# Optimization experiments

Measured on AMD Instinct MI355X. Metric: run time of the kernel, lower is better.

The kernel has to match this reference:

```python
import jax, jax.numpy as jnp
import numpy as np
from jax import lax

HEADS = 8
DIM_HEAD = 64
INNER = HEADS * DIM_HEAD  # 512
DIM = 256
TOP_K = 512  # top_k=-1 -> Lk // heads = 4096 // 8
LN_EPS = 1e-5


def chan_ln(x, g, b):
    # LayerNorm over channel dim (axis=1) of [b,c,D,H,W]
    mu = jnp.mean(x, axis=1, keepdims=True)
    var = jnp.mean((x - mu) ** 2, axis=1, keepdims=True)
    xn = (x - mu) * lax.rsqrt(var + LN_EPS)
    return xn * g[None, :, None, None, None] + b[None, :, None, None, None]


def l1_cdist(K, Q):
    # K: [B,N,D], Q: [B,M,D] -> [B,N,M]; scan over feature dim to avoid a [B,N,M,D] intermediate
    Kt = jnp.moveaxis(K, -1, 0)  # [D,B,N]
    Qt = jnp.moveaxis(Q, -1, 0)  # [D,B,M]
    acc0 = jnp.zeros((K.shape[0], K.shape[1], Q.shape[1]), K.dtype)
    def step(acc, kq):
        kd, qd = kq
        return acc + jnp.abs(kd[:, :, None] - qd[:, None, :]), None
    acc, _ = lax.scan(step, acc0, (Kt, Qt))
    return acc


def l2norm_ax(t, axis):
    n = jnp.sqrt(jnp.sum(t * t, axis=axis, keepdims=True))
    return t / jnp.maximum(n, 1e-12)


def setup_inputs() -> dict:
    key = jax.random.key(0)
    ks = jax.random.split(key, 12)
    b, Dq, Hq, Wq = 2, 16, 32, 32
    Dc, Hc, Wc = 16, 16, 16
    Lk = Dc * Hc * Wc  # 4096
    return {
        "query_source": jax.random.normal(ks[0], (b, DIM, Dq, Hq, Wq), jnp.float32),
        "context": jax.random.normal(ks[1], (b, DIM, Dc, Hc, Wc), jnp.float32),
        "rand_idx": jax.random.randint(ks[2], (b * HEADS, TOP_K), 0, 4096),
        "g_ctx": jnp.ones((DIM,), jnp.float32),
        "b_ctx": jnp.zeros((DIM,), jnp.float32),
        "g_qs": jnp.ones((DIM,), jnp.float32),
        "b_qs": jnp.zeros((DIM,), jnp.float32),
        "w_kv": jax.random.normal(ks[3], (2 * INNER, DIM), jnp.float32) * 0.02,
        "w_q": jax.random.normal(ks[4], (INNER, DIM), jnp.float32) * 0.02,
        "w_out": jax.random.normal(ks[5], (DIM, INNER), jnp.float32) * 0.02,
        "g_out": jnp.ones((DIM,), jnp.float32),
        "b_out": jnp.zeros((DIM,), jnp.float32),
        "gamma": jnp.full((1,), 0.5, jnp.float32),
    }


def reference(query_source, context, rand_idx, g_ctx, b_ctx, g_qs, b_qs,
              w_kv, w_q, w_out, g_out, b_out, gamma):
    b, c, Dq, Hq, Wq = query_source.shape
    Lq = Dq * Hq * Wq
    Lk = context.shape[2] * context.shape[3] * context.shape[4]

    ctx = chan_ln(context, g_ctx, b_ctx)
    qsn = chan_ln(query_source, g_qs, b_qs)

    # 1x1x1 convs == channel matmuls
    kv = jnp.einsum('oc,bcdhw->bodhw', w_kv, ctx)
    k, v = jnp.split(kv, 2, axis=1)
    q = jnp.einsum('oc,bcdhw->bodhw', w_q, qsn)

    def fold(t):  # [b, inner, ...] -> [b, heads, dim_head, L]
        return t.reshape(t.shape[0], HEADS, DIM_HEAD, -1)
    q, k, v = fold(q), fold(k), fold(v)
    # l2norm over dim_head channels (torch dim=1 after (b h) fold)
    q = l2norm_ax(q, 2)
    k = l2norm_ax(k, 2)
    # -> [b, heads, L, dim_head]
    q = jnp.swapaxes(q, 2, 3)
    k = jnp.swapaxes(k, 2, 3)
    v = jnp.swapaxes(v, 2, 3)

    BH = b * HEADS
    qf = q.reshape(BH, Lq, DIM_HEAD)
    kf = k.reshape(BH, Lk, DIM_HEAD)
    vf = v.reshape(BH, Lk, DIM_HEAD)

    # random-query-anchored token pruning
    Q_small = jnp.take_along_axis(qf, rand_idx[:, :, None], axis=1)  # [BH, TOP_K, dh]
    dist = l1_cdist(kf, Q_small)                                     # [BH, Lk, TOP_K]
    min_d = jnp.min(dist, axis=2)                                    # [BH, Lk]
    _, idx = lax.top_k(-min_d, TOP_K)                                # smallest distances
    ks_sel = jnp.take_along_axis(kf, idx[:, :, None], axis=1)        # [BH, TOP_K, dh]
    vs_sel = jnp.take_along_axis(vf, idx[:, :, None], axis=1)

    ks4 = ks_sel.reshape(b, HEADS, TOP_K, DIM_HEAD)
    vs4 = vs_sel.reshape(b, HEADS, TOP_K, DIM_HEAD)

    # SDPA with scale=1.0, no dropout (eval)
    scores = jnp.einsum('bhqd,bhkd->bhqk', q, ks4)
    attn = jax.nn.softmax(scores, axis=-1)
    out = jnp.einsum('bhqk,bhkd->bhqd', attn, vs4)  # [b,H,Lq,dh]

    out = out.reshape(b, HEADS, Dq, Hq, Wq, DIM_HEAD)
    out = jnp.transpose(out, (0, 1, 5, 2, 3, 4)).reshape(b, INNER, Dq, Hq, Wq)
    out = jnp.einsum('oc,bcdhw->bodhw', w_out, out)
    out = chan_ln(out, g_out, b_out)
    return gamma[0] * out + query_source
```

## Files before the change

### kernel.cpp

```cpp
#include <hip/hip_runtime.h>
#include <hip/hip_bf16.h>
#include <math.h>

#define DIMC  256
#define HEADS 8
#define DH    64
#define INNER 512
#define TOPK  512
#define LQ    16384
#define LKE   4096
#define NB    2
#define NBH   16

typedef __attribute__((ext_vector_type(8))) short bf16x8;
typedef __attribute__((ext_vector_type(4))) float f32x4;
typedef __attribute__((ext_vector_type(16))) unsigned u32x16;

__device__ __forceinline__ unsigned short f2bf(float f) {
    unsigned u = __float_as_uint(f);
    u += 0x7FFFu + ((u >> 16) & 1u);
    return (unsigned short)(u >> 16);
}
__device__ __forceinline__ float bf2f(unsigned short b) {
    return __uint_as_float(((unsigned)b) << 16);
}
__device__ __forceinline__ f32x4 mfma16(bf16x8 a, bf16x8 b, f32x4 c) {
    return __builtin_amdgcn_mfma_f32_16x16x32_bf16(a, b, c, 0, 0, 0);
}
__device__ __forceinline__ unsigned f2q16(float v) {
    return (unsigned)((int)rintf(v * 32000.0f) + 32768) & 0xFFFFu;
}

__global__ void stats_kernel(const float* __restrict__ x, float* __restrict__ mu,
                             float* __restrict__ rs, int L, int total) {
    int idx = blockIdx.x * 256 + threadIdx.x;
    if (idx >= total) return;
    int b = idx / L, l = idx - b * L;
    const float* p = x + (size_t)b * DIMC * L + l;
    float s = 0.f, sq = 0.f;
    for (int c = 0; c < DIMC; c++) {
        float v = p[(size_t)c * L];
        s += v; sq += v * v;
    }
    float m = s * (1.0f / DIMC);
    float var = fmaxf(sq * (1.0f / DIMC) - m * m, 0.f);
    mu[idx] = m;
    rs[idx] = rsqrtf(var + 1e-5f);
}

template<bool WRITELO>
__global__ __launch_bounds__(256) void ln_transpose_kernel(
    const float* __restrict__ x, const float* __restrict__ mu, const float* __restrict__ rs,
    const float* __restrict__ g, const float* __restrict__ beta, int L,
    unsigned short* __restrict__ xhi, unsigned short* __restrict__ xlo) {
    int lt = blockIdx.x, ct = blockIdx.y, b = blockIdx.z;
    int l0 = lt * 64, c0 = ct * 64;
    int t = threadIdx.x;
    __shared__ float T[64][65];
#pragma unroll
    for (int r = 0; r < 16; r++) {
        int f = r * 256 + t;
        int l = f & 63, c = f >> 6;
        int loc = b * L + l0 + l;
        float v = x[((size_t)b * DIMC + c0 + c) * L + l0 + l];
        T[c][l] = (v - mu[loc]) * rs[loc] * g[c0 + c] + beta[c0 + c];
    }
    __syncthreads();
#pragma unroll
    for (int r = 0; r < 16; r++) {
        int f = r * 256 + t;
        int c = f & 63, l = f >> 6;
        float v = T[c][l];
        unsigned short hi = f2bf(v);
        size_t di = ((size_t)b * L + l0 + l) * DIMC + c0 + c;
        xhi[di] = hi;
        if (WRITELO) xlo[di] = f2bf(v - bf2f(hi));
    }
}

template<int MODE>
__global__ __launch_bounds__(256) void gemm_mfma_kernel(
    const float* __restrict__ wmat,
    const unsigned short* __restrict__ xhi, const unsigned short* __restrict__ xlo,
    void* __restrict__ dst0, void* __restrict__ dst1, void* __restrict__ dst2) {
    constexpr int K = (MODE == 2) ? 512 : 256;
    constexpr int N = (MODE == 0) ? LKE : LQ;
    constexpr bool MAYSPLIT = (MODE == 0);
    int n0 = blockIdx.x * 128;
    int by = blockIdx.y;
    int bb = blockIdx.z;
    int t = threadIdx.x, w = t >> 6, lane = t & 63;
    int wm = w >> 1, wn = w & 1;
    int lanelo = lane & 15, lanehi = lane >> 4;

    __shared__ __align__(16) char Wh[16384];
    __shared__ __align__(16) char Xh[16384];
    __shared__ __align__(16) char Wl[MAYSPLIT ? 16384 : 16];
    __shared__ __align__(16) char Xl[MAYSPLIT ? 16384 : 16];

    bool split = MAYSPLIT && (by < 4);

    const float* wsrc = wmat + (size_t)by * 128 * K;
    const unsigned short* xsh = xhi + ((size_t)bb * N + n0) * K;
    const unsigned short* xsl = xlo + ((size_t)bb * N + n0) * K;

    f32x4 acc[4][4];
#pragma unroll
    for (int mi = 0; mi < 4; mi++)
#pragma unroll
        for (int ni = 0; ni < 4; ni++) acc[mi][ni] = (f32x4){0.f, 0.f, 0.f, 0.f};

    for (int k0 = 0; k0 < K; k0 += 64) {
        if (k0) __syncthreads();
#pragma unroll
        for (int gg = 0; gg < 4; gg++) {
            int e = gg * 2048 + t * 8;
            int row = e >> 6, kc = e & 63;
            const float* wp = wsrc + (size_t)row * K + k0 + kc;
            bf16x8 hi, lo;
#pragma unroll
            for (int i = 0; i < 8; i++) {
                float v = wp[i];
                unsigned short h = f2bf(v);
                hi[i] = (short)h;
                if (MAYSPLIT) lo[i] = (short)f2bf(v - bf2f(h));
            }
            int off = (row * 128 + kc * 2) ^ ((row & 7) << 4);
            *(bf16x8*)(Wh + off) = hi;
            *(bf16x8*)(Xh + off) = *(const bf16x8*)(xsh + (size_t)row * K + k0 + kc);
            if (split) {
                *(bf16x8*)(Wl + off) = lo;
                *(bf16x8*)(Xl + off) = *(const bf16x8*)(xsl + (size_t)row * K + k0 + kc);
            }
        }
        __syncthreads();
#pragma unroll
        for (int kk = 0; kk < 2; kk++) {
            bf16x8 ah[4], bh_[4];
#pragma unroll
            for (int mi = 0; mi < 4; mi++) {
                int row = wm * 64 + mi * 16 + lanelo;
                int off = (row * 128 + kk * 64 + lanehi * 16) ^ ((row & 7) << 4);
                ah[mi] = *(const bf16x8*)(Wh + off);
            }
#pragma unroll
            for (int ni = 0; ni < 4; ni++) {
                int row = wn * 64 + ni * 16 + lanelo;
                int off = (row * 128 + kk * 64 + lanehi * 16) ^ ((row & 7) << 4);
                bh_[ni] = *(const bf16x8*)(Xh + off);
            }
#pragma unroll
            for (int mi = 0; mi < 4; mi++)
#pragma unroll
                for (int ni = 0; ni < 4; ni++)
                    acc[mi][ni] = mfma16(ah[mi], bh_[ni], acc[mi][ni]);
            if (split) {
                bf16x8 al[4], bl_[4];
#pragma unroll
                for (int mi = 0; mi < 4; mi++) {
                    int row = wm * 64 + mi * 16 + lanelo;
                    int off = (row * 128 + kk * 64 + lanehi * 16) ^ ((row & 7) << 4);
                    al[mi] = *(const bf16x8*)(Wl + off);
                }
#pragma unroll
                for (int ni = 0; ni < 4; ni++) {
                    int row = wn * 64 + ni * 16 + lanelo;
                    int off = (row * 128 + kk * 64 + lanehi * 16) ^ ((row & 7) << 4);
                    bl_[ni] = *(const bf16x8*)(Xl + off);
                }
#pragma unroll
                for (int mi = 0; mi < 4; mi++)
#pragma unroll
                    for (int ni = 0; ni < 4; ni++) {
                        acc[mi][ni] = mfma16(ah[mi], bl_[ni], acc[mi][ni]);
                        acc[mi][ni] = mfma16(al[mi], bh_[ni], acc[mi][ni]);
                    }
            }
        }
    }

    bool donorm = (MODE == 1) || (MODE == 0 && by < 4);
    float inv[4];
    if (donorm) {
#pragma unroll
        for (int ni = 0; ni < 4; ni++) {
            float s = 0.f;
#pragma unroll
            for (int mi = 0; mi < 4; mi++)
#pragma unroll
                for (int rg = 0; rg < 4; rg++) s += acc[mi][ni][rg] * acc[mi][ni][rg];
            s += __shfl_xor(s, 16);
            s += __shfl_xor(s, 32);
            inv[ni] = 1.0f / fmaxf(sqrtf(s), 1e-12f);
        }
    }
#pragma unroll
    for (int mi = 0; mi < 4; mi++) {
        int rowg = by * 128 + wm * 64 + mi * 16 + lanehi * 4;
#pragma unroll
        for (int ni = 0; ni < 4; ni++) {
            int l = n0 + wn * 64 + ni * 16 + lanelo;
            if (MODE == 0) {
                bool isk = rowg < 512;
                float sc = isk ? inv[ni] : 1.0f;
                int h = (rowg >> 6) & 7, d0 = rowg & 63;
                float4 v = make_float4(acc[mi][ni][0] * sc, acc[mi][ni][1] * sc,
                                       acc[mi][ni][2] * sc, acc[mi][ni][3] * sc);
                float* dp = isk ? (float*)dst0 : (float*)dst1;
                size_t base = ((size_t)(bb * HEADS + h) * LKE + l) * 64 + d0;
                *(float4*)&dp[base] = v;
                if (isk) {
                    uint2 pk;
                    pk.x = f2q16(v.x) | (f2q16(v.y) << 16);
                    pk.y = f2q16(v.z) | (f2q16(v.w) << 16);
                    *(uint2*)&((unsigned*)dst2)[(((size_t)(bb * HEADS + h) * LKE + l) * 64 + d0) / 2] = pk;
                }
            } else if (MODE == 1) {
                int h = rowg >> 6, d0 = rowg & 63;
                ushort4 u;
                u.x = f2bf(acc[mi][ni][0] * inv[ni]);
                u.y = f2bf(acc[mi][ni][1] * inv[ni]);
                u.z = f2bf(acc[mi][ni][2] * inv[ni]);
                u.w = f2bf(acc[mi][ni][3] * inv[ni]);
                unsigned short* qp = (unsigned short*)dst0;
                *(ushort4*)&qp[((size_t)(bb * HEADS + h) * LQ + l) * 64 + d0] = u;
            } else {
                float4 v = make_float4(acc[mi][ni][0], acc[mi][ni][1],
                                       acc[mi][ni][2], acc[mi][ni][3]);
                float* pp = (float*)dst0;
                *(float4*)&pp[((size_t)bb * LQ + l) * 256 + rowg] = v;
            }
        }
    }
}

__global__ __launch_bounds__(256) void qsample_kernel(
    const float* __restrict__ x, const float* __restrict__ mu, const float* __restrict__ rs,
    const float* __restrict__ g, const float* __restrict__ beta,
    const float* __restrict__ w, const int* __restrict__ ridx,
    unsigned* __restrict__ Qint) {
    int lt = blockIdx.x, bh = blockIdx.y;
    int b = bh >> 3, h = bh & 7;
    int t = threadIdx.x, tx = t & 15, ty = t >> 4;
    __shared__ float Ws[64][33];
    __shared__ float Xs[32][65];
    __shared__ float Cs[64][65];
    __shared__ float nf[64];
    __shared__ int lidx[64];
    if (t < 64) lidx[t] = ridx[bh * TOPK + lt * 64 + t];
    __syncthreads();
    float acc[4][4];
#pragma unroll
    for (int a = 0; a < 4; a++)
#pragma unroll
        for (int c2 = 0; c2 < 4; c2++) acc[a][c2] = 0.f;
    for (int kc = 0; kc < DIMC; kc += 32) {
#pragma unroll
        for (int r = 0; r < 8; r++) {
            int f = r * 256 + t;
            int oi = f >> 5, kj = f & 31;
            Ws[oi][kj] = w[(size_t)(h * 64 + oi) * DIMC + kc + kj];
        }
#pragma unroll
        for (int r = 0; r < 8; r++) {
            int f = r * 256 + t;
            int kj = f >> 6, lj = f & 63;
            int l = lidx[lj];
            int loc = b * LQ + l;
            float v = x[(size_t)b * DIMC * LQ + (size_t)(kc + kj) * LQ + l];
            Xs[kj][lj] = (v - mu[loc]) * rs[loc] * g[kc + kj] + beta[kc + kj];
        }
        __syncthreads();
#pragma unroll
        for (int kj = 0; kj < 32; kj++) {
            float wr[4], xr[4];
#pragma unroll
            for (int a = 0; a < 4; a++) wr[a] = Ws[ty * 4 + a][kj];
#pragma unroll
            for (int c2 = 0; c2 < 4; c2++) xr[c2] = Xs[kj][tx * 4 + c2];
#pragma unroll
            for (int a = 0; a < 4; a++)
#pragma unroll
                for (int c2 = 0; c2 < 4; c2++) acc[a][c2] += wr[a] * xr[c2];
        }
        __syncthreads();
    }
#pragma unroll
    for (int a = 0; a < 4; a++)
#pragma unroll
        for (int c2 = 0; c2 < 4; c2++) Cs[ty * 4 + a][tx * 4 + c2] = acc[a][c2];
    __syncthreads();
    if (t < 64) {
        float sq = 0.f;
        for (int o = 0; o < 64; o++) { float v = Cs[o][t]; sq += v * v; }
        nf[t] = 1.0f / fmaxf(sqrtf(sq), 1e-12f);
    }
    __syncthreads();
#pragma unroll
    for (int r = 0; r < 8; r++) {
        int f = r * 256 + t;
        int dp = f & 31, lj = f >> 5;
        float v0 = Cs[dp * 2][lj] * nf[lj];
        float v1 = Cs[dp * 2 + 1][lj] * nf[lj];
        Qint[((size_t)bh * TOPK + (size_t)lt * 64 + lj) * 32 + dp] =
            f2q16(v0) | (f2q16(v1) << 16);
    }
}

__global__ __launch_bounds__(256) __attribute__((amdgpu_waves_per_eu(4, 4)))
void cdist_sad_kernel(
    const unsigned* __restrict__ kint,
    const unsigned* __restrict__ Qint,
    unsigned* __restrict__ min_d4) {
    int bh = blockIdx.y;
    int key = blockIdx.x * 256 + threadIdx.x;
    int qz = blockIdx.z;
    const unsigned* kp = kint + ((size_t)bh * LKE + key) * 32;
    unsigned k[32];
#pragma unroll
    for (int d8 = 0; d8 < 8; d8++) {
        uint4 v = *(const uint4*)(kp + d8 * 4);
        k[d8 * 4 + 0] = v.x; k[d8 * 4 + 1] = v.y;
        k[d8 * 4 + 2] = v.z; k[d8 * 4 + 3] = v.w;
    }
#pragma unroll
    for (int d = 0; d < 32; d++) asm volatile("" : "+v"(k[d]));

    unsigned long long qaddr = (unsigned long long)(const void*)
        (Qint + ((size_t)bh * TOPK + (size_t)qz * (TOPK / 4)) * 32);
    u32x16 qa0, qa1, qb0, qb1;
    asm volatile(
        "s_load_dwordx16 %0, %2, 0x00\n\t"
        "s_load_dwordx16 %1, %2, 0x40"
        : "=s"(qa0), "=s"(qa1) : "s"(qaddr));
    unsigned best = 0xFFFFFFFFu;

#define S1(ACC, KK, QQ) asm("v_sad_u16 %0, %1, %2, %0" : "+v"(ACC) : "v"(KK), "s"(QQ));
#define S16(QV, KB) \
    S1(a0, k[KB + 0], QV[0])  S1(a1, k[KB + 1], QV[1]) \
    S1(a2, k[KB + 2], QV[2])  S1(a3, k[KB + 3], QV[3]) \
    S1(a0, k[KB + 4], QV[4])  S1(a1, k[KB + 5], QV[5]) \
    S1(a2, k[KB + 6], QV[6])  S1(a3, k[KB + 7], QV[7]) \
    S1(a0, k[KB + 8], QV[8])  S1(a1, k[KB + 9], QV[9]) \
    S1(a2, k[KB + 10], QV[10]) S1(a3, k[KB + 11], QV[11]) \
    S1(a0, k[KB + 12], QV[12]) S1(a1, k[KB + 13], QV[13]) \
    S1(a2, k[KB + 14], QV[14]) S1(a3, k[KB + 15], QV[15])

    for (int qi = 0; qi < TOPK / 4; qi += 2) {
        asm volatile(
            "s_load_dwordx16 %0, %2, 0x80\n\t"
            "s_load_dwordx16 %1, %2, 0xc0"
            : "=s"(qb0), "=s"(qb1) : "s"(qaddr));
        asm volatile("s_waitcnt lgkmcnt(2)" : "+s"(qa0), "+s"(qa1));
        {
            unsigned a0 = 0, a1 = 0, a2 = 0, a3 = 0;
            S16(qa0, 0) S16(qa1, 16)
            best = min(best, (a0 + a1) + (a2 + a3));
        }
        qaddr += 256;
        asm volatile(
            "s_load_dwordx16 %0, %2, 0x00\n\t"
            "s_load_dwordx16 %1, %2, 0x40"
            : "=s"(qa0), "=s"(qa1) : "s"(qaddr));
        asm volatile("s_waitcnt lgkmcnt(2)" : "+s"(qb0), "+s"(qb1));
        {
            unsigned a0 = 0, a1 = 0, a2 = 0, a3 = 0;
            S16(qb0, 0) S16(qb1, 16)
            best = min(best, (a0 + a1) + (a2 + a3));
        }
    }
#undef S16
#undef S1
    min_d4[((size_t)qz * NBH + bh) * LKE + key] = best;
}

__global__ void select_topk_kernel(const unsigned* __restrict__ min_d4, int* __restrict__ isel) {
    int bh = blockIdx.x;
    int t = threadIdx.x;
    __shared__ unsigned su[LKE];
    __shared__ int hist[256];
    __shared__ int sb[2];
    for (int i = t; i < LKE; i += 256) {
        unsigned a = min(min_d4[(size_t)bh * LKE + i],
                         min_d4[(size_t)(NBH + bh) * LKE + i]);
        unsigned b = min(min_d4[(size_t)(2 * NBH + bh) * LKE + i],
                         min_d4[(size_t)(3 * NBH + bh) * LKE + i]);
        su[i] = min(a, b);
    }
    unsigned prefix = 0, mask = 0;
    int need = TOPK;
    for (int shift = 24; shift >= 0; shift -= 8) {
        hist[t] = 0;
        __syncthreads();
        for (int i = t; i < LKE; i += 256) {
            unsigned u = su[i];
            if ((u & mask) == prefix) atomicAdd(&hist[(u >> shift) & 255], 1);
        }
        __syncthreads();
        if (t == 0) {
            int c = 0, bsel = 0;
            for (; bsel < 255; bsel++) {
                if (c + hist[bsel] >= need) break;
                c += hist[bsel];
            }
            sb[0] = bsel; sb[1] = need - c;
        }
        __syncthreads();
        prefix |= ((unsigned)sb[0]) << shift;
        mask |= (255u << shift);
        need = sb[1];
        __syncthreads();
    }
    if (t < 64) {
        int pos = 0, eqseen = 0;
        unsigned long long lanem1 = (t == 0) ? 0ull : ((1ull << t) - 1ull);
        for (int i0 = 0; i0 < LKE; i0 += 64) {
            unsigned u = su[i0 + t];
            bool lt = (u < prefix);
            bool eq = (u == prefix);
            unsigned long long be = __ballot(eq);
            int eqbefore = __popcll(be & lanem1);
            bool take = lt || (eq && (eqseen + eqbefore) < need);
            unsigned long long bt = __ballot(take);
            if (take) isel[bh * TOPK + pos + __popcll(bt & lanem1)] = i0 + t;
            pos += __popcll(bt);
            eqseen += __popcll(be);
        }
    }
}

__global__ void gather_k_kernel(const float* __restrict__ kf, const int* __restrict__ isel,
                                unsigned short* __restrict__ kselh) {
    int idx = blockIdx.x * 256 + threadIdx.x;
    int d = idx & 63;
    int ti = (idx >> 6) & (TOPK - 1);
    int bh = idx >> 15;
    int row = isel[bh * TOPK + ti];
    kselh[idx] = f2bf(kf[((size_t)bh * LKE + row) * 64 + d]);
}

__global__ __launch_bounds__(256) void gather_vT_kernel(
    const float* __restrict__ vf, const int* __restrict__ isel,
    unsigned short* __restrict__ vTh) {
    int bh = blockIdx.y, kc = blockIdx.x * 64;
    int t = threadIdx.x;
    __shared__ float T[64][65];
#pragma unroll
    for (int r = 0; r < 4; r++) {
        int c = r * 256 + t;
        int row = c >> 4, c4 = c & 15;
        int krow = isel[bh * TOPK + kc + row];
        float4 v = *(const float4*)(vf + ((size_t)bh * LKE + krow) * 64 + c4 * 4);
        T[row][c4 * 4 + 0] = v.x; T[row][c4 * 4 + 1] = v.y;
        T[row][c4 * 4 + 2] = v.z; T[row][c4 * 4 + 3] = v.w;
    }
    __syncthreads();
#pragma unroll
    for (int r = 0; r < 16; r++) {
        int f = r * 256 + t;
        int d = f >> 6, key = f & 63;
        vTh[(size_t)bh * 64 * TOPK + (size_t)d * TOPK + kc + key] = f2bf(T[key][d]);
    }
}

__global__ __launch_bounds__(256) void attn_mfma_kernel(
    const unsigned short* __restrict__ qh,
    const unsigned short* __restrict__ kselh,
    const unsigned short* __restrict__ vTh,
    unsigned short* __restrict__ afT) {
    int bh = blockIdx.y, rt = blockIdx.x;
    int bq = bh >> 3, h = bh & 7;
    int t = threadIdx.x, w = t >> 6, lane = t & 63;
    __shared__ unsigned short Ks[2][64 * 64];
    __shared__ unsigned short Vts[2][64 * 64];
    __shared__ unsigned short Ps[4][2][16 * 64];

    const unsigned short* qb = qh + ((size_t)bh * LQ + (size_t)rt * 128) * 64;
    const unsigned short* kb = kselh + (size_t)bh * TOPK * 64;
    const unsigned short* vb = vTh + (size_t)bh * 64 * TOPK;

    int lanelo = lane & 15, lanehi = lane >> 4;

    int row0s = t >> 3, c80 = t & 7;
    int row1s = 32 + (t >> 3), c81 = t & 7;
    int offs0 = (row0s * 128 + c80 * 16) ^ ((row0s & 7) << 4);
    int offs1 = (row1s * 128 + c81 * 16) ^ ((row1s & 7) << 4);

    bf16x8 qfrag[2][2];
#pragma unroll
    for (int s = 0; s < 2; s++)
#pragma unroll
        for (int kk = 0; kk < 2; kk++) {
            int row = s * 64 + w * 16 + lanelo;
            qfrag[s][kk] = *(const bf16x8*)(qb + (size_t)row * 64 + kk * 32 + lanehi * 8);
        }

    {
        *(bf16x8*)((char*)Ks[0] + offs0) = *(const bf16x8*)(kb + row0s * 64 + c80 * 8);
        *(bf16x8*)((char*)Ks[0] + offs1) = *(const bf16x8*)(kb + row1s * 64 + c81 * 8);
        *(bf16x8*)((char*)Vts[0] + offs0) = *(const bf16x8*)(vb + row0s * TOPK + c80 * 8);
        *(bf16x8*)((char*)Vts[0] + offs1) = *(const bf16x8*)(vb + row1s * TOPK + c81 * 8);
    }
    __syncthreads();

    f32x4 o[2][4];
#pragma unroll
    for (int s = 0; s < 2; s++)
#pragma unroll
        for (int m = 0; m < 4; m++) o[s][m] = (f32x4){0.f, 0.f, 0.f, 0.f};
    float part[2][4] = {{0.f, 0.f, 0.f, 0.f}, {0.f, 0.f, 0.f, 0.f}};
    int cur = 0;

    for (int ch = 0; ch < 8; ch++) {
        bf16x8 knx0, knx1, vnx0, vnx1;
        if (ch < 7) {
            int kc0 = (ch + 1) * 64;
            knx0 = *(const bf16x8*)(kb + (kc0 + row0s) * 64 + c80 * 8);
            knx1 = *(const bf16x8*)(kb + (kc0 + row1s) * 64 + c81 * 8);
            vnx0 = *(const bf16x8*)(vb + row0s * TOPK + kc0 + c80 * 8);
            vnx1 = *(const bf16x8*)(vb + row1s * TOPK + kc0 + c81 * 8);
        }
        bf16x8 kfr[4][2];
#pragma unroll
        for (int n = 0; n < 4; n++)
#pragma unroll
            for (int kk = 0; kk < 2; kk++) {
                int row = n * 16 + lanelo;
                kfr[n][kk] = *(const bf16x8*)((char*)Ks[cur] +
                    ((row * 128 + kk * 64 + lanehi * 16) ^ ((row & 7) << 4)));
            }
#pragma unroll
        for (int s = 0; s < 2; s++) {
            f32x4 sv[4];
#pragma unroll
            for (int n = 0; n < 4; n++) {
                sv[n] = (f32x4){0.f, 0.f, 0.f, 0.f};
#pragma unroll
                for (int kk = 0; kk < 2; kk++)
                    sv[n] = mfma16(qfrag[s][kk], kfr[n][kk], sv[n]);
            }
            unsigned short* pw = Ps[w][s];
#pragma unroll
            for (int n = 0; n < 4; n++) {
#pragma unroll
                for (int rg = 0; rg < 4; rg++) {
                    float p = __expf(sv[n][rg]);
                    part[s][rg] += p;
                    int row = lanehi * 4 + rg, col = n * 16 + lanelo;
                    *(unsigned short*)((char*)pw +
                        ((row * 128 + col * 2) ^ ((row & 7) << 4))) = f2bf(p);
                }
            }
        }
        bf16x8 vfr[4][2];
#pragma unroll
        for (int m = 0; m < 4; m++)
#pragma unroll
            for (int kk = 0; kk < 2; kk++) {
                int row = m * 16 + lanelo;
                vfr[m][kk] = *(const bf16x8*)((char*)Vts[cur] +
                    ((row * 128 + kk * 64 + lanehi * 16) ^ ((row & 7) << 4)));
            }
#pragma unroll
        for (int s = 0; s < 2; s++) {
            bf16x8 pfrag[2];
#pragma unroll
            for (int kk = 0; kk < 2; kk++) {
                int row = lanelo;
                pfrag[kk] = *(const bf16x8*)((char*)Ps[w][s] +
                    ((row * 128 + kk * 64 + lanehi * 16) ^ ((row & 7) << 4)));
            }
#pragma unroll
            for (int m = 0; m < 4; m++)
#pragma unroll
                for (int kk = 0; kk < 2; kk++)
                    o[s][m] = mfma16(pfrag[kk], vfr[m][kk], o[s][m]);
        }
        if (ch < 7) {
            *(bf16x8*)((char*)Ks[cur ^ 1] + offs0) = knx0;
            *(bf16x8*)((char*)Ks[cur ^ 1] + offs1) = knx1;
            *(bf16x8*)((char*)Vts[cur ^ 1] + offs0) = vnx0;
            *(bf16x8*)((char*)Vts[cur ^ 1] + offs1) = vnx1;
        }
        __syncthreads();
        cur ^= 1;
    }
#pragma unroll
    for (int s = 0; s < 2; s++) {
#pragma unroll
        for (int rg = 0; rg < 4; rg++) {
            float v = part[s][rg];
            v += __shfl_xor(v, 1); v += __shfl_xor(v, 2);
            v += __shfl_xor(v, 4); v += __shfl_xor(v, 8);
            float invs = 1.0f / v;
            int l = rt * 128 + s * 64 + w * 16 + lanehi * 4 + rg;
            size_t base = ((size_t)bq * LQ + l) * 512 + h * 64 + lanelo;
#pragma unroll
            for (int m = 0; m < 4; m++)
                afT[base + m * 16] = f2bf(o[s][m][rg] * invs);
        }
    }
}

__global__ void stats_loc_kernel(const float* __restrict__ pre, float* __restrict__ mu,
                                 float* __restrict__ rs) {
    int t = threadIdx.x;
    int grp = t >> 4, ln = t & 15;
    int loc = blockIdx.x * 16 + grp;
    const float4* p = (const float4*)(pre + (size_t)loc * 256);
    float s = 0.f, sq = 0.f;
#pragma unroll
    for (int i = 0; i < 4; i++) {
        float4 v = p[ln + i * 16];
        s += v.x + v.y + v.z + v.w;
        sq += v.x * v.x + v.y * v.y + v.z * v.z + v.w * v.w;
    }
#pragma unroll
    for (int d = 1; d < 16; d <<= 1) {
        s += __shfl_xor(s, d);
        sq += __shfl_xor(sq, d);
    }
    if (ln == 0) {
        float m = s * (1.0f / 256.0f);
        float var = fmaxf(sq * (1.0f / 256.0f) - m * m, 0.f);
        mu[loc] = m;
        rs[loc] = rsqrtf(var + 1e-5f);
    }
}

__global__ __launch_bounds__(256) void final_kernel(
    const float* __restrict__ pre, const float* __restrict__ mu,
    const float* __restrict__ rs, const float* __restrict__ g,
    const float* __restrict__ beta, const float* __restrict__ gamma,
    const float* __restrict__ qs_in, float* __restrict__ out) {
    int lt = blockIdx.x, ot = blockIdx.y, b = blockIdx.z;
    int l0 = lt * 64, o0 = ot * 64;
    int t = threadIdx.x;
    __shared__ float T[64][65];
    float gm = gamma[0];
#pragma unroll
    for (int r = 0; r < 16; r++) {
        int f = r * 256 + t;
        int o = f & 63, l = f >> 6;
        int loc = b * LQ + l0 + l;
        float v = pre[(size_t)loc * 256 + o0 + o];
        T[o][l] = ((v - mu[loc]) * rs[loc] * g[o0 + o] + beta[o0 + o]) * gm;
    }
    __syncthreads();
#pragma unroll
    for (int r = 0; r < 16; r++) {
        int f = r * 256 + t;
        int l = f & 63, o = f >> 6;
        size_t oi = ((size_t)(b * DIMC + o0 + o)) * LQ + l0 + l;
        out[oi] = T[o][l] + qs_in[oi];
    }
}

extern "C" void kernel_launch(void* const* d_in, const int* in_sizes, int n_in,
                              void* d_out, int out_size, void* d_ws, size_t ws_size,
                              hipStream_t stream) {
    const float* qs_in = (const float*)d_in[0];
    const float* ctx   = (const float*)d_in[1];
    const int*   ridx  = (const int*)d_in[2];
    const float* g_ctx = (const float*)d_in[3];
    const float* b_ctx = (const float*)d_in[4];
    const float* g_qs  = (const float*)d_in[5];
    const float* b_qs  = (const float*)d_in[6];
    const float* w_kv  = (const float*)d_in[7];
    const float* w_q   = (const float*)d_in[8];
    const float* w_out = (const float*)d_in[9];
    const float* g_out = (const float*)d_in[10];
    const float* b_out = (const float*)d_in[11];
    const float* gamma = (const float*)d_in[12];
    float* out = (float*)d_out;

    char* ws = (char*)d_ws;
    size_t off = 0;
    auto alloc = [&](size_t bytes) { char* p = ws + off; off += (bytes + 255) & ~(size_t)255; return p; };

    float*          kf    = (float*)alloc((size_t)NBH * LKE * 64 * 4);
    float*          vf    = (float*)alloc((size_t)NBH * LKE * 64 * 4);
    unsigned*       kint  = (unsigned*)alloc((size_t)NBH * LKE * 32 * 4);
    unsigned short* qh    = (unsigned short*)alloc((size_t)NBH * LQ * 64 * 2);
    char*           uni   = alloc((size_t)NB * LQ * INNER * 2);
    unsigned short* ctxT_hi = (unsigned short*)(uni);
    unsigned short* ctxT_lo = (unsigned short*)(uni + (size_t)NB * LKE * DIMC * 2);
    unsigned short* qsT_hi  = (unsigned short*)(uni + (size_t)2 * NB * LKE * DIMC * 2);
    unsigned short* afT     = (unsigned short*)(uni);

    unsigned*       Qint  = (unsigned*)alloc((size_t)NBH * TOPK * 32 * 4);
    unsigned short* kselh = (unsigned short*)alloc((size_t)NBH * TOPK * 64 * 2);
    unsigned short* vTh   = (unsigned short*)alloc((size_t)NBH * 64 * TOPK * 2);
    float*          pre   = (float*)alloc((size_t)NB * LQ * DIMC * 4);
    unsigned*       min_d4= (unsigned*)alloc((size_t)4 * NBH * LKE * 4);
    float*          mu_c  = (float*)alloc(NB * LKE * 4);
    float*          rs_c  = (float*)alloc(NB * LKE * 4);
    float*          mu_q  = (float*)alloc(NB * LQ * 4);
    float*          rs_q  = (float*)alloc(NB * LQ * 4);
    float*          mu_o  = (float*)alloc(NB * LQ * 4);
    float*          rs_o  = (float*)alloc(NB * LQ * 4);
    int*            isel  = (int*)alloc(NBH * TOPK * 4);

    stats_kernel<<<(NB * LKE + 255) / 256, 256, 0, stream>>>(ctx, mu_c, rs_c, LKE, NB * LKE);
    stats_kernel<<<(NB * LQ + 255) / 256, 256, 0, stream>>>(qs_in, mu_q, rs_q, LQ, NB * LQ);
    ln_transpose_kernel<true><<<dim3(LKE / 64, DIMC / 64, NB), 256, 0, stream>>>(
        ctx, mu_c, rs_c, g_ctx, b_ctx, LKE, ctxT_hi, ctxT_lo);
    ln_transpose_kernel<false><<<dim3(LQ / 64, DIMC / 64, NB), 256, 0, stream>>>(
        qs_in, mu_q, rs_q, g_qs, b_qs, LQ, qsT_hi, nullptr);
    gemm_mfma_kernel<0><<<dim3(LKE / 128, 8, NB), 256, 0, stream>>>(
        w_kv, ctxT_hi, ctxT_lo, kf, vf, kint);
    gemm_mfma_kernel<1><<<dim3(LQ / 128, 4, NB), 256, 0, stream>>>(
        w_q, qsT_hi, qsT_hi, qh, nullptr, nullptr);
    qsample_kernel<<<dim3(TOPK / 64, NBH), 256, 0, stream>>>(
        qs_in, mu_q, rs_q, g_qs, b_qs, w_q, ridx, Qint);
    cdist_sad_kernel<<<dim3(LKE / 256, NBH, 4), 256, 0, stream>>>(kint, Qint, min_d4);
    select_topk_kernel<<<NBH, 256, 0, stream>>>(min_d4, isel);
    gather_k_kernel<<<(NBH * TOPK * 64) / 256, 256, 0, stream>>>(kf, isel, kselh);
    gather_vT_kernel<<<dim3(TOPK / 64, NBH), 256, 0, stream>>>(vf, isel, vTh);
    attn_mfma_kernel<<<dim3(LQ / 128, NBH), 256, 0, stream>>>(qh, kselh, vTh, afT);
    gemm_mfma_kernel<2><<<dim3(LQ / 128, 2, NB), 256, 0, stream>>>(
        w_out, afT, afT, pre, nullptr, nullptr);
    stats_loc_kernel<<<(NB * LQ) / 16, 256, 0, stream>>>(pre, mu_o, rs_o);
    final_kernel<<<dim3(LQ / 64, DIMC / 64, NB), 256, 0, stream>>>(
        pre, mu_o, rs_o, g_out, b_out, gamma, qs_in, out);
}
```

Before: 341.3 us.

## Merge stats and gather launches, parallel scan in top-k, truncate softmax probs

Merges the two LayerNorm statistics kernels into one launch and the K and V gather kernels into one kernel that loads the selected row indices once into shared memory. In the top-k radix select, the serial single-thread histogram scan is replaced with a block-wide Hillis-Steele prefix scan. In attention, probabilities are converted to bf16 by truncation instead of round-to-nearest, and the row sum now accumulates the truncated values so it matches what goes into the PV product. The aim is fewer launches and less serial work, at the cost of slightly different rounding and more barriers in the scan.

Result: faster. 310.8 us (-9.0%).

```diff
diff --git a/kernel.cpp b/kernel.cpp
--- a/kernel.cpp
+++ b/kernel.cpp
@@ -31,11 +31,14 @@
     return (unsigned)((int)rintf(v * 32000.0f) + 32768) & 0xFFFFu;
 }
 
-__global__ void stats_kernel(const float* __restrict__ x, float* __restrict__ mu,
-                             float* __restrict__ rs, int L, int total) {
+__global__ void stats_all_kernel(const float* __restrict__ ctx, const float* __restrict__ qs,
+                                 float* __restrict__ mu_c, float* __restrict__ rs_c,
+                                 float* __restrict__ mu_q, float* __restrict__ rs_q) {
     int idx = blockIdx.x * 256 + threadIdx.x;
-    if (idx >= total) return;
-    int b = idx / L, l = idx - b * L;
+    const float* x; float* mu; float* rs; int L; int li;
+    if (idx < NB * LKE) { x = ctx; mu = mu_c; rs = rs_c; L = LKE; li = idx; }
+    else { li = idx - NB * LKE; if (li >= NB * LQ) return; x = qs; mu = mu_q; rs = rs_q; L = LQ; }
+    int b = li / L, l = li - b * L;
     const float* p = x + (size_t)b * DIMC * L + l;
     float s = 0.f, sq = 0.f;
     for (int c = 0; c < DIMC; c++) {
@@ -44,8 +47,8 @@
     }
     float m = s * (1.0f / DIMC);
     float var = fmaxf(sq * (1.0f / DIMC) - m * m, 0.f);
-    mu[idx] = m;
-    rs[idx] = rsqrtf(var + 1e-5f);
+    mu[li] = m;
+    rs[li] = rsqrtf(var + 1e-5f);
 }
 
 template<bool WRITELO>
@@ -379,6 +382,7 @@
     int t = threadIdx.x;
     __shared__ unsigned su[LKE];
     __shared__ int hist[256];
+    __shared__ int scan[256];
     __shared__ int sb[2];
     for (int i = t; i < LKE; i += 256) {
         unsigned a = min(min_d4[(size_t)bh * LKE + i],
@@ -397,13 +401,19 @@
             if ((u & mask) == prefix) atomicAdd(&hist[(u >> shift) & 255], 1);
         }
         __syncthreads();
-        if (t == 0) {
-            int c = 0, bsel = 0;
-            for (; bsel < 255; bsel++) {
-                if (c + hist[bsel] >= need) break;
-                c += hist[bsel];
-            }
-            sb[0] = bsel; sb[1] = need - c;
+        scan[t] = hist[t];
+        __syncthreads();
+#pragma unroll
+        for (int d = 1; d < 256; d <<= 1) {
+            int v = (t >= d) ? scan[t - d] : 0;
+            __syncthreads();
+            scan[t] += v;
+            __syncthreads();
+        }
+        int excl = (t == 0) ? 0 : scan[t - 1];
+        if (scan[t] >= need && excl < need) {
+            sb[0] = t;
+            sb[1] = need - excl;
         }
         __syncthreads();
         prefix |= ((unsigned)sb[0]) << shift;
@@ -429,28 +439,28 @@
     }
 }
 
-__global__ void gather_k_kernel(const float* __restrict__ kf, const int* __restrict__ isel,
-                                unsigned short* __restrict__ kselh) {
-    int idx = blockIdx.x * 256 + threadIdx.x;
-    int d = idx & 63;
-    int ti = (idx >> 6) & (TOPK - 1);
-    int bh = idx >> 15;
-    int row = isel[bh * TOPK + ti];
-    kselh[idx] = f2bf(kf[((size_t)bh * LKE + row) * 64 + d]);
-}
-
-__global__ __launch_bounds__(256) void gather_vT_kernel(
-    const float* __restrict__ vf, const int* __restrict__ isel,
-    unsigned short* __restrict__ vTh) {
+__global__ __launch_bounds__(256) void gather_kv_kernel(
+    const float* __restrict__ kf, const float* __restrict__ vf,
+    const int* __restrict__ isel,
+    unsigned short* __restrict__ kselh, unsigned short* __restrict__ vTh) {
     int bh = blockIdx.y, kc = blockIdx.x * 64;
     int t = threadIdx.x;
     __shared__ float T[64][65];
+    __shared__ int rows[64];
+    if (t < 64) rows[t] = isel[bh * TOPK + kc + t];
+    __syncthreads();
+#pragma unroll
+    for (int r = 0; r < 16; r++) {
+        int f = r * 256 + t;
+        int key = f >> 6, d = f & 63;
+        kselh[((size_t)bh * TOPK + kc + key) * 64 + d] =
+            f2bf(kf[((size_t)bh * LKE + rows[key]) * 64 + d]);
+    }
 #pragma unroll
     for (int r = 0; r < 4; r++) {
         int c = r * 256 + t;
         int row = c >> 4, c4 = c & 15;
-        int krow = isel[bh * TOPK + kc + row];
-        float4 v = *(const float4*)(vf + ((size_t)bh * LKE + krow) * 64 + c4 * 4);
+        float4 v = *(const float4*)(vf + ((size_t)bh * LKE + rows[row]) * 64 + c4 * 4);
         T[row][c4 * 4 + 0] = v.x; T[row][c4 * 4 + 1] = v.y;
         T[row][c4 * 4 + 2] = v.z; T[row][c4 * 4 + 3] = v.w;
     }
@@ -545,10 +555,11 @@
 #pragma unroll
                 for (int rg = 0; rg < 4; rg++) {
                     float p = __expf(sv[n][rg]);
-                    part[s][rg] += p;
+                    unsigned short ph = (unsigned short)(__float_as_uint(p) >> 16);
+                    part[s][rg] += bf2f(ph);
                     int row = lanehi * 4 + rg, col = n * 16 + lanelo;
                     *(unsigned short*)((char*)pw +
-                        ((row * 128 + col * 2) ^ ((row & 7) << 4))) = f2bf(p);
+                        ((row * 128 + col * 2) ^ ((row & 7) << 4))) = ph;
                 }
             }
         }
@@ -701,8 +712,8 @@
     float*          rs_o  = (float*)alloc(NB * LQ * 4);
     int*            isel  = (int*)alloc(NBH * TOPK * 4);
 
-    stats_kernel<<<(NB * LKE + 255) / 256, 256, 0, stream>>>(ctx, mu_c, rs_c, LKE, NB * LKE);
-    stats_kernel<<<(NB * LQ + 255) / 256, 256, 0, stream>>>(qs_in, mu_q, rs_q, LQ, NB * LQ);
+    stats_all_kernel<<<(NB * (LKE + LQ)) / 256, 256, 0, stream>>>(
+        ctx, qs_in, mu_c, rs_c, mu_q, rs_q);
     ln_transpose_kernel<true><<<dim3(LKE / 64, DIMC / 64, NB), 256, 0, stream>>>(
         ctx, mu_c, rs_c, g_ctx, b_ctx, LKE, ctxT_hi, ctxT_lo);
     ln_transpose_kernel<false><<<dim3(LQ / 64, DIMC / 64, NB), 256, 0, stream>>>(
@@ -715,8 +726,7 @@
         qs_in, mu_q, rs_q, g_qs, b_qs, w_q, ridx, Qint);
     cdist_sad_kernel<<<dim3(LKE / 256, NBH, 4), 256, 0, stream>>>(kint, Qint, min_d4);
     select_topk_kernel<<<NBH, 256, 0, stream>>>(min_d4, isel);
-    gather_k_kernel<<<(NBH * TOPK * 64) / 256, 256, 0, stream>>>(kf, isel, kselh);
-    gather_vT_kernel<<<dim3(TOPK / 64, NBH), 256, 0, stream>>>(vf, isel, vTh);
+    gather_kv_kernel<<<dim3(TOPK / 64, NBH), 256, 0, stream>>>(kf, vf, isel, kselh, vTh);
     attn_mfma_kernel<<<dim3(LQ / 128, NBH), 256, 0, stream>>>(qh, kselh, vTh, afT);
     gemm_mfma_kernel<2><<<dim3(LQ / 128, 2, NB), 256, 0, stream>>>(
         w_out, afT, afT, pre, nullptr, nullptr);
```
